# Optimization experiments

Hardware: AMD Instinct MI355X
Metric: run time of the kernel (lower is better)

Reference implementation:

```python
import jax, jax.numpy as jnp
import numpy as np

EPS = 1e-4


def _linear_scan(a, b):
    # y_t = a_t * y_{t-1} + b_t ; a: [L], b: [L, d]
    def combine(c1, c2):
        a1, b1 = c1
        a2, b2 = c2
        return a1 * a2, a2[..., None] * b1 + b2
    _, y = jax.lax.associative_scan(combine, (a, b))
    return y


def setup_inputs() -> dict:
    key = jax.random.key(0)
    k1, k2, k3 = jax.random.split(key, 3)
    L_inner, d, n_seqs = 131072, 512, 8
    h_flat = jax.random.normal(k1, (L_inner, d), dtype=jnp.float32)
    p_selected_flat = jax.random.uniform(k2, (L_inner,), dtype=jnp.float32)
    # outer stream: alternating boundary mask -> cumsum-1 indexes stay in [0, L_inner-1]
    b_flat = jnp.tile(jnp.array([1, 0], dtype=jnp.int32), L_inner)  # [2*L_inner]
    h_seq_idx = jnp.sort(jax.random.randint(k3, (1, L_inner), 0, n_seqs)).astype(jnp.int32)
    return {"h_flat": h_flat, "b_flat": b_flat,
            "p_selected_flat": p_selected_flat, "h_seq_idx": h_seq_idx}


def reference(h_flat, b_flat, p_selected_flat, h_seq_idx):
    # dt derivation: p clamped, dt = -log(1-p); x = h / dt (cast round-trip as in torch)
    p = jnp.clip(p_selected_flat.astype(jnp.float32), EPS, 1.0 - EPS)
    dt = -jnp.log1p(-p)                                   # [L]
    x = (h_flat.astype(jnp.float32) / dt[:, None]).astype(h_flat.dtype).astype(jnp.float32)
    # mamba_chunk_scan_combined with A=-1, B=p, C=1, dstate=1 reduces to:
    #   state_t = exp(-dt_t) * state_{t-1} + dt_t * p_t * x_t ; y_t = state_t
    # with state reset at seq_idx segment boundaries.
    seq = h_seq_idx[0]
    start = jnp.concatenate([jnp.array([True]), seq[1:] != seq[:-1]])
    a = jnp.where(start, 0.0, jnp.exp(-dt))               # decay (== 1-p), reset at starts
    b = (dt * p)[:, None] * x                             # [L, d] input term (== p*h)
    z_bar = _linear_scan(a, b).astype(h_flat.dtype)       # [L_inner, d]
    # dechunk expand: each outer token reads the state of its latest chunk
    idx = jnp.cumsum(b_flat) - 1                          # [L_outer]
    return z_bar[idx]
```

## Files before the change

### kernel.cpp

```cpp
#include <hip/hip_runtime.h>
#include <math.h>

#define EPSV 1e-4f
#define SCHUNK 64

__device__ __forceinline__ float agent_load_f(const float* p) {
    return __hip_atomic_load(p, __ATOMIC_RELAXED, __HIP_MEMORY_SCOPE_AGENT);
}
__device__ __forceinline__ void agent_store_f(float* p, float v) {
    __hip_atomic_store(p, v, __ATOMIC_RELAXED, __HIP_MEMORY_SCOPE_AGENT);
}
__device__ __forceinline__ int agent_load_i(const int* p) {
    return __hip_atomic_load(p, __ATOMIC_RELAXED, __HIP_MEMORY_SCOPE_AGENT);
}
__device__ __forceinline__ void agent_store_i(int* p, int v) {
    __hip_atomic_store(p, v, __ATOMIC_RELAXED, __HIP_MEMORY_SCOPE_AGENT);
}

__global__ void clear_kernel(int* __restrict__ flags, int n) {
    int i = blockIdx.x * blockDim.x + threadIdx.x;
    if (i < n) flags[i] = 0;
}

__global__ void scan_sum_kernel(const int* __restrict__ b, int n,
                                int* __restrict__ bsum) {
    __shared__ int red[256];
    int tid = threadIdx.x;
    int base = blockIdx.x * 1024 + tid * 4;
    int s = 0;
#pragma unroll
    for (int k = 0; k < 4; ++k) {
        int j = base + k;
        if (j < n) s += b[j];
    }
    red[tid] = s;
    __syncthreads();
    for (int off = 128; off > 0; off >>= 1) {
        if (tid < off) red[tid] += red[tid + off];
        __syncthreads();
    }
    if (tid == 0) bsum[blockIdx.x] = red[0];
}

__global__ void scan_offsets_kernel(const int* __restrict__ bsum,
                                    int* __restrict__ boff, int nb) {
    __shared__ int sh[1024];
    int i = threadIdx.x;
    int v = (i < nb) ? bsum[i] : 0;
    sh[i] = v;
    __syncthreads();
    for (int off = 1; off < 1024; off <<= 1) {
        int t = sh[i];
        if (i >= off) t += sh[i - off];
        __syncthreads();
        sh[i] = t;
        __syncthreads();
    }
    if (i < nb) boff[i] = sh[i] - v;
}

__global__ void scan_emit_kernel(const int* __restrict__ b, int n,
                                 const int* __restrict__ boff,
                                 int* __restrict__ sidx, int L, int Louter) {
    __shared__ int red[256];
    int tid = threadIdx.x;
    int base = blockIdx.x * 1024 + tid * 4;
    int v[4];
    int s = 0;
#pragma unroll
    for (int k = 0; k < 4; ++k) {
        int j = base + k;
        v[k] = (j < n) ? b[j] : 0;
        s += v[k];
    }
    red[tid] = s;
    __syncthreads();
    for (int off = 1; off < 256; off <<= 1) {
        int t = red[tid];
        if (tid >= off) t += red[tid - off];
        __syncthreads();
        red[tid] = t;
        __syncthreads();
    }
    int cum = red[tid] - s + boff[blockIdx.x];
#pragma unroll
    for (int k = 0; k < 4; ++k) {
        int j = base + k;
        if (j < n) {
            cum += v[k];
            if (v[k] > 0) {
                int t = cum - 1;
                if (t >= 0 && t < L) sidx[t] = j;
            }
        }
    }
    if (base == 0 && blockIdx.x == 0) sidx[L] = Louter;
}

__global__ __launch_bounds__(512, 4) void scan_lookback_kernel(
        const float* __restrict__ h,
        const float* __restrict__ psel,
        const int* __restrict__ seq,
        const int* __restrict__ sidx,
        float* __restrict__ out,
        float* __restrict__ aggE,
        float* __restrict__ aggP,
        int* __restrict__ flags,
        int L, int d, int Louter, int NC) {
    __shared__ float sh_a[SCHUNK];
    __shared__ float sh_p[SCHUNK];
    __shared__ int   sh_j[SCHUNK + 1];
    __shared__ int   sh_g;
    __shared__ float sh_Pown;
    __shared__ float sh_Pbr;

    const int tid = threadIdx.x;
    if (tid == 0) sh_g = atomicAdd(&flags[NC], 1);
    __syncthreads();
    const int g  = sh_g;
    const int t0 = g * SCHUNK;
    const int nt = min(SCHUNK, L - t0);

    if (tid < nt) {
        int t = t0 + tid;
        float p = psel[t];
        p = fminf(fmaxf(p, EPSV), 1.0f - EPSV);
        bool start = (t == 0) || (seq[t] != seq[t - 1]);
        sh_a[tid] = start ? 0.0f : (1.0f - p);
        sh_p[tid] = p;
    }
    if (tid <= nt) sh_j[tid] = sidx[t0 + tid];
    __syncthreads();

    if (tid < 64) {
        float v = (tid < nt) ? sh_a[tid] : 1.0f;
#pragma unroll
        for (int m = 1; m < 64; m <<= 1) v *= __shfl_xor(v, m);
        if (tid == 0) sh_Pown = v;
    }

    const int c = tid;
    const float* __restrict__ hp = h + (size_t)t0 * d + c;

    float st = 0.0f;
    const bool full = (nt == SCHUNK);
    if (full) {
#pragma unroll
        for (int grp = 0; grp < SCHUNK / 8; ++grp) {
            float hb[8];
#pragma unroll
            for (int k = 0; k < 8; ++k)
                hb[k] = hp[(size_t)(grp * 8 + k) * d];
#pragma unroll
            for (int k = 0; k < 8; ++k) {
                int t = grp * 8 + k;
                st = fmaf(sh_a[t], st, sh_p[t] * hb[k]);
            }
        }
    } else {
        for (int t = 0; t < nt; ++t)
            st = fmaf(sh_a[t], st, sh_p[t] * hp[(size_t)t * d]);
    }

    agent_store_f(&aggE[(size_t)g * d + c], st);
    __syncthreads();
    if (tid == 0) {
        agent_store_f(&aggP[g], sh_Pown);
        asm volatile("s_waitcnt vmcnt(0)" ::: "memory");
        agent_store_i(&flags[g], 1);
    }

    float carry = 0.0f;
    float prodAcc = 1.0f;
    for (int i = g - 1; i >= 0; --i) {
        if (tid == 0) {
            while (agent_load_i(&flags[i]) == 0) __builtin_amdgcn_s_sleep(1);
            sh_Pbr = agent_load_f(&aggP[i]);
        }
        __syncthreads();
        float Pi = sh_Pbr;
        carry = fmaf(prodAcc, agent_load_f(&aggE[(size_t)i * d + c]), carry);
        prodAcc *= Pi;
        __syncthreads();
        if (prodAcc == 0.0f) break;
    }

    float s2 = carry;
    if (full) {
#pragma unroll
        for (int grp = 0; grp < SCHUNK / 8; ++grp) {
            float hb[8];
#pragma unroll
            for (int k = 0; k < 8; ++k)
                hb[k] = hp[(size_t)(grp * 8 + k) * d];
#pragma unroll
            for (int k = 0; k < 8; ++k) {
                int t = grp * 8 + k;
                s2 = fmaf(sh_a[t], s2, sh_p[t] * hb[k]);
                int j0 = max(sh_j[t], 0);
                int j1 = min(sh_j[t + 1], Louter);
                for (int j = j0; j < j1; ++j)
                    __builtin_nontemporal_store(s2, out + (size_t)j * d + c);
            }
        }
    } else {
        for (int t = 0; t < nt; ++t) {
            s2 = fmaf(sh_a[t], s2, sh_p[t] * hp[(size_t)t * d]);
            int j0 = max(sh_j[t], 0);
            int j1 = min(sh_j[t + 1], Louter);
            for (int j = j0; j < j1; ++j)
                out[(size_t)j * d + c] = s2;
        }
    }
}

extern "C" void kernel_launch(void* const* d_in, const int* in_sizes, int n_in,
                              void* d_out, int out_size, void* d_ws, size_t ws_size,
                              hipStream_t stream) {
    const float* h     = (const float*)d_in[0];
    const int*   bflat = (const int*)d_in[1];
    const float* psel  = (const float*)d_in[2];
    const int*   seq   = (const int*)d_in[3];
    float* out = (float*)d_out;

    const int L      = in_sizes[2];
    const int Louter = in_sizes[1];
    const int d      = in_sizes[0] / L;

    const int NC = (L + SCHUNK - 1) / SCHUNK;
    const int nb = (Louter + 1023) / 1024;

    char* ws = (char*)d_ws;
    size_t off = 0;
    auto alloc = [&](size_t bytes) -> void* {
        void* p = ws + off;
        off = (off + bytes + 255) & ~(size_t)255;
        return p;
    };
    float* aggE  = (float*)alloc((size_t)NC * d * 4);
    float* aggP  = (float*)alloc((size_t)NC * 4);
    int*   flags = (int*)alloc((size_t)(NC + 1) * 4);
    int*   bsum  = (int*)alloc((size_t)nb * 4);
    int*   boff  = (int*)alloc((size_t)nb * 4);
    int*   sidx  = (int*)alloc((size_t)(L + 1) * 4);
    (void)ws_size;

    clear_kernel<<<(NC + 1 + 255) / 256, 256, 0, stream>>>(flags, NC + 1);

    scan_sum_kernel<<<nb, 256, 0, stream>>>(bflat, Louter, bsum);
    scan_offsets_kernel<<<1, 1024, 0, stream>>>(bsum, boff, nb);
    scan_emit_kernel<<<nb, 256, 0, stream>>>(bflat, Louter, boff, sidx, L, Louter);

    scan_lookback_kernel<<<NC, d, 0, stream>>>(h, psel, seq, sidx, out,
                                               aggE, aggP, flags,
                                               L, d, Louter, NC);
}
```

Measured before the change: 190.0 us.

## Vectorize lookback scan to float4 per thread and fuse index scan kernels

```diff
diff --git a/kernel.cpp b/kernel.cpp
--- a/kernel.cpp
+++ b/kernel.cpp
@@ -4,6 +4,8 @@
 #define EPSV 1e-4f
 #define SCHUNK 64
 
+typedef float f32x4 __attribute__((ext_vector_type(4)));
+
 __device__ __forceinline__ float agent_load_f(const float* p) {
     return __hip_atomic_load(p, __ATOMIC_RELAXED, __HIP_MEMORY_SCOPE_AGENT);
 }
@@ -15,6 +17,14 @@
 }
 __device__ __forceinline__ void agent_store_i(int* p, int v) {
     __hip_atomic_store(p, v, __ATOMIC_RELAXED, __HIP_MEMORY_SCOPE_AGENT);
+}
+__device__ __forceinline__ f32x4 agent_load_f4(const float* p) {
+    f32x4 r;
+    r.x = agent_load_f(p + 0);
+    r.y = agent_load_f(p + 1);
+    r.z = agent_load_f(p + 2);
+    r.w = agent_load_f(p + 3);
+    return r;
 }
 
 __global__ void clear_kernel(int* __restrict__ flags, int n) {
@@ -22,49 +32,17 @@
     if (i < n) flags[i] = 0;
 }
 
-__global__ void scan_sum_kernel(const int* __restrict__ b, int n,
-                                int* __restrict__ bsum) {
+__global__ __launch_bounds__(256) void sidx_kernel(
+        const int* __restrict__ b, int n,
+        int* __restrict__ bsum,
+        int* __restrict__ flags2,
+        int* __restrict__ sidx, int L, int Louter) {
     __shared__ int red[256];
-    int tid = threadIdx.x;
-    int base = blockIdx.x * 1024 + tid * 4;
-    int s = 0;
-#pragma unroll
-    for (int k = 0; k < 4; ++k) {
-        int j = base + k;
-        if (j < n) s += b[j];
-    }
-    red[tid] = s;
-    __syncthreads();
-    for (int off = 128; off > 0; off >>= 1) {
-        if (tid < off) red[tid] += red[tid + off];
-        __syncthreads();
-    }
-    if (tid == 0) bsum[blockIdx.x] = red[0];
-}
-
-__global__ void scan_offsets_kernel(const int* __restrict__ bsum,
-                                    int* __restrict__ boff, int nb) {
-    __shared__ int sh[1024];
-    int i = threadIdx.x;
-    int v = (i < nb) ? bsum[i] : 0;
-    sh[i] = v;
-    __syncthreads();
-    for (int off = 1; off < 1024; off <<= 1) {
-        int t = sh[i];
-        if (i >= off) t += sh[i - off];
-        __syncthreads();
-        sh[i] = t;
-        __syncthreads();
-    }
-    if (i < nb) boff[i] = sh[i] - v;
-}
-
-__global__ void scan_emit_kernel(const int* __restrict__ b, int n,
-                                 const int* __restrict__ boff,
-                                 int* __restrict__ sidx, int L, int Louter) {
-    __shared__ int red[256];
-    int tid = threadIdx.x;
-    int base = blockIdx.x * 1024 + tid * 4;
+    __shared__ int red2[256];
+    const int tid = threadIdx.x;
+    const int bid = blockIdx.x;
+    const int base = bid * 1024 + tid * 4;
+
     int v[4];
     int s = 0;
 #pragma unroll
@@ -82,7 +60,25 @@
         red[tid] = t;
         __syncthreads();
     }
-    int cum = red[tid] - s + boff[blockIdx.x];
+    if (tid == 255) {
+        agent_store_i(&bsum[bid], red[255]);
+        asm volatile("s_waitcnt vmcnt(0)" ::: "memory");
+        agent_store_i(&flags2[bid], 1);
+    }
+    int mysum = 0;
+    if (tid < bid) {
+        while (agent_load_i(&flags2[tid]) == 0) __builtin_amdgcn_s_sleep(1);
+        mysum = agent_load_i(&bsum[tid]);
+    }
+    red2[tid] = mysum;
+    __syncthreads();
+    for (int off = 128; off > 0; off >>= 1) {
+        if (tid < off) red2[tid] += red2[tid + off];
+        __syncthreads();
+    }
+    const int boff = red2[0];
+
+    int cum = red[tid] - s + boff;
 #pragma unroll
     for (int k = 0; k < 4; ++k) {
         int j = base + k;
@@ -94,10 +90,10 @@
             }
         }
     }
-    if (base == 0 && blockIdx.x == 0) sidx[L] = Louter;
-}
-
-__global__ __launch_bounds__(512, 4) void scan_lookback_kernel(
+    if (tid == 0 && bid == 0) sidx[L] = Louter;
+}
+
+__global__ __launch_bounds__(128, 4) void scan_lookback_kernel(
         const float* __restrict__ h,
         const float* __restrict__ psel,
         const int* __restrict__ seq,
@@ -139,30 +135,44 @@
         if (tid == 0) sh_Pown = v;
     }
 
-    const int c = tid;
-    const float* __restrict__ hp = h + (size_t)t0 * d + c;
-
-    float st = 0.0f;
+    const int c0 = tid * 4;
+    const float* __restrict__ hp = h + (size_t)t0 * d + c0;
+
+    f32x4 st = {0.f, 0.f, 0.f, 0.f};
     const bool full = (nt == SCHUNK);
     if (full) {
 #pragma unroll
         for (int grp = 0; grp < SCHUNK / 8; ++grp) {
-            float hb[8];
+            f32x4 hb[8];
 #pragma unroll
             for (int k = 0; k < 8; ++k)
-                hb[k] = hp[(size_t)(grp * 8 + k) * d];
+                hb[k] = *(const f32x4*)(hp + (size_t)(grp * 8 + k) * d);
 #pragma unroll
             for (int k = 0; k < 8; ++k) {
                 int t = grp * 8 + k;
-                st = fmaf(sh_a[t], st, sh_p[t] * hb[k]);
+                float at = sh_a[t], pt = sh_p[t];
+                st.x = fmaf(at, st.x, pt * hb[k].x);
+                st.y = fmaf(at, st.y, pt * hb[k].y);
+                st.z = fmaf(at, st.z, pt * hb[k].z);
+                st.w = fmaf(at, st.w, pt * hb[k].w);
             }
         }
     } else {
-        for (int t = 0; t < nt; ++t)
-            st = fmaf(sh_a[t], st, sh_p[t] * hp[(size_t)t * d]);
-    }
-
-    agent_store_f(&aggE[(size_t)g * d + c], st);
+        for (int t = 0; t < nt; ++t) {
+            f32x4 h4 = *(const f32x4*)(hp + (size_t)t * d);
+            float at = sh_a[t], pt = sh_p[t];
+            st.x = fmaf(at, st.x, pt * h4.x);
+            st.y = fmaf(at, st.y, pt * h4.y);
+            st.z = fmaf(at, st.z, pt * h4.z);
+            st.w = fmaf(at, st.w, pt * h4.w);
+        }
+    }
+
+    float* ep = aggE + (size_t)g * d + c0;
+    agent_store_f(ep + 0, st.x);
+    agent_store_f(ep + 1, st.y);
+    agent_store_f(ep + 2, st.z);
+    agent_store_f(ep + 3, st.w);
     __syncthreads();
     if (tid == 0) {
         agent_store_f(&aggP[g], sh_Pown);
@@ -170,7 +180,7 @@
         agent_store_i(&flags[g], 1);
     }
 
-    float carry = 0.0f;
+    f32x4 carry = {0.f, 0.f, 0.f, 0.f};
     float prodAcc = 1.0f;
     for (int i = g - 1; i >= 0; --i) {
         if (tid == 0) {
@@ -179,37 +189,50 @@
         }
         __syncthreads();
         float Pi = sh_Pbr;
-        carry = fmaf(prodAcc, agent_load_f(&aggE[(size_t)i * d + c]), carry);
+        f32x4 E = agent_load_f4(aggE + (size_t)i * d + c0);
+        carry.x = fmaf(prodAcc, E.x, carry.x);
+        carry.y = fmaf(prodAcc, E.y, carry.y);
+        carry.z = fmaf(prodAcc, E.z, carry.z);
+        carry.w = fmaf(prodAcc, E.w, carry.w);
         prodAcc *= Pi;
         __syncthreads();
         if (prodAcc == 0.0f) break;
     }
 
-    float s2 = carry;
+    f32x4 s2 = carry;
     if (full) {
 #pragma unroll
         for (int grp = 0; grp < SCHUNK / 8; ++grp) {
-            float hb[8];
+            f32x4 hb[8];
 #pragma unroll
             for (int k = 0; k < 8; ++k)
-                hb[k] = hp[(size_t)(grp * 8 + k) * d];
+                hb[k] = *(const f32x4*)(hp + (size_t)(grp * 8 + k) * d);
 #pragma unroll
             for (int k = 0; k < 8; ++k) {
                 int t = grp * 8 + k;
-                s2 = fmaf(sh_a[t], s2, sh_p[t] * hb[k]);
+                float at = sh_a[t], pt = sh_p[t];
+                s2.x = fmaf(at, s2.x, pt * hb[k].x);
+                s2.y = fmaf(at, s2.y, pt * hb[k].y);
+                s2.z = fmaf(at, s2.z, pt * hb[k].z);
+                s2.w = fmaf(at, s2.w, pt * hb[k].w);
                 int j0 = max(sh_j[t], 0);
                 int j1 = min(sh_j[t + 1], Louter);
                 for (int j = j0; j < j1; ++j)
-                    __builtin_nontemporal_store(s2, out + (size_t)j * d + c);
+                    __builtin_nontemporal_store(s2, (f32x4*)(out + (size_t)j * d + c0));
             }
         }
     } else {
         for (int t = 0; t < nt; ++t) {
-            s2 = fmaf(sh_a[t], s2, sh_p[t] * hp[(size_t)t * d]);
+            f32x4 h4 = *(const f32x4*)(hp + (size_t)t * d);
+            float at = sh_a[t], pt = sh_p[t];
+            s2.x = fmaf(at, s2.x, pt * h4.x);
+            s2.y = fmaf(at, s2.y, pt * h4.y);
+            s2.z = fmaf(at, s2.z, pt * h4.z);
+            s2.w = fmaf(at, s2.w, pt * h4.w);
             int j0 = max(sh_j[t], 0);
             int j1 = min(sh_j[t + 1], Louter);
             for (int j = j0; j < j1; ++j)
-                out[(size_t)j * d + c] = s2;
+                *(f32x4*)(out + (size_t)j * d + c0) = s2;
         }
     }
 }
@@ -237,21 +260,19 @@
         off = (off + bytes + 255) & ~(size_t)255;
         return p;
     };
-    float* aggE  = (float*)alloc((size_t)NC * d * 4);
-    float* aggP  = (float*)alloc((size_t)NC * 4);
-    int*   flags = (int*)alloc((size_t)(NC + 1) * 4);
-    int*   bsum  = (int*)alloc((size_t)nb * 4);
-    int*   boff  = (int*)alloc((size_t)nb * 4);
-    int*   sidx  = (int*)alloc((size_t)(L + 1) * 4);
+    float* aggE   = (float*)alloc((size_t)NC * d * 4);
+    float* aggP   = (float*)alloc((size_t)NC * 4);
+    int*   flags  = (int*)alloc((size_t)(NC + 1 + nb) * 4);
+    int*   bsum   = (int*)alloc((size_t)nb * 4);
+    int*   sidx   = (int*)alloc((size_t)(L + 1) * 4);
+    int*   flags2 = flags + NC + 1;
     (void)ws_size;
 
-    clear_kernel<<<(NC + 1 + 255) / 256, 256, 0, stream>>>(flags, NC + 1);
-
-    scan_sum_kernel<<<nb, 256, 0, stream>>>(bflat, Louter, bsum);
-    scan_offsets_kernel<<<1, 1024, 0, stream>>>(bsum, boff, nb);
-    scan_emit_kernel<<<nb, 256, 0, stream>>>(bflat, Louter, boff, sidx, L, Louter);
-
-    scan_lookback_kernel<<<NC, d, 0, stream>>>(h, psel, seq, sidx, out,
-                                               aggE, aggP, flags,
-                                               L, d, Louter, NC);
-}
+    clear_kernel<<<(NC + 1 + nb + 255) / 256, 256, 0, stream>>>(flags, NC + 1 + nb);
+
+    sidx_kernel<<<nb, 256, 0, stream>>>(bflat, Louter, bsum, flags2, sidx, L, Louter);
+
+    scan_lookback_kernel<<<NC, d / 4, 0, stream>>>(h, psel, seq, sidx, out,
+                                                   aggE, aggP, flags,
+                                                   L, d, Louter, NC);
+}
```

Measured after the change: 215.0 us. 13.2% more time.

## Shrink scan chunk and keep local states in registers to skip second h pass

Applied to the files above, without the earlier changes.

```diff
diff --git a/kernel.cpp b/kernel.cpp
--- a/kernel.cpp
+++ b/kernel.cpp
@@ -2,7 +2,7 @@
 #include <math.h>
 
 #define EPSV 1e-4f
-#define SCHUNK 64
+#define SCHUNK 16
 
 __device__ __forceinline__ float agent_load_f(const float* p) {
     return __hip_atomic_load(p, __ATOMIC_RELAXED, __HIP_MEMORY_SCOPE_AGENT);
@@ -97,7 +97,7 @@
     if (base == 0 && blockIdx.x == 0) sidx[L] = Louter;
 }
 
-__global__ __launch_bounds__(512, 4) void scan_lookback_kernel(
+__global__ __launch_bounds__(512, 8) void scan_lookback_kernel(
         const float* __restrict__ h,
         const float* __restrict__ psel,
         const int* __restrict__ seq,
@@ -109,9 +109,9 @@
         int L, int d, int Louter, int NC) {
     __shared__ float sh_a[SCHUNK];
     __shared__ float sh_p[SCHUNK];
+    __shared__ float sh_A[SCHUNK];
     __shared__ int   sh_j[SCHUNK + 1];
     __shared__ int   sh_g;
-    __shared__ float sh_Pown;
     __shared__ float sh_Pbr;
 
     const int tid = threadIdx.x;
@@ -131,31 +131,28 @@
     }
     if (tid <= nt) sh_j[tid] = sidx[t0 + tid];
     __syncthreads();
-
-    if (tid < 64) {
-        float v = (tid < nt) ? sh_a[tid] : 1.0f;
-#pragma unroll
-        for (int m = 1; m < 64; m <<= 1) v *= __shfl_xor(v, m);
-        if (tid == 0) sh_Pown = v;
-    }
+    if (tid < nt) {
+        float prod = 1.0f;
+        for (int u = 0; u <= tid; ++u) prod *= sh_a[u];
+        sh_A[tid] = prod;
+    }
+    __syncthreads();
 
     const int c = tid;
     const float* __restrict__ hp = h + (size_t)t0 * d + c;
-
+    const bool full = (nt == SCHUNK);
+
+    float z[SCHUNK];
     float st = 0.0f;
-    const bool full = (nt == SCHUNK);
     if (full) {
-#pragma unroll
-        for (int grp = 0; grp < SCHUNK / 8; ++grp) {
-            float hb[8];
-#pragma unroll
-            for (int k = 0; k < 8; ++k)
-                hb[k] = hp[(size_t)(grp * 8 + k) * d];
-#pragma unroll
-            for (int k = 0; k < 8; ++k) {
-                int t = grp * 8 + k;
-                st = fmaf(sh_a[t], st, sh_p[t] * hb[k]);
-            }
+        float hb[SCHUNK];
+#pragma unroll
+        for (int t = 0; t < SCHUNK; ++t)
+            hb[t] = __builtin_nontemporal_load(hp + (size_t)t * d);
+#pragma unroll
+        for (int t = 0; t < SCHUNK; ++t) {
+            st = fmaf(sh_a[t], st, sh_p[t] * hb[t]);
+            z[t] = st;
         }
     } else {
         for (int t = 0; t < nt; ++t)
@@ -165,7 +162,7 @@
     agent_store_f(&aggE[(size_t)g * d + c], st);
     __syncthreads();
     if (tid == 0) {
-        agent_store_f(&aggP[g], sh_Pown);
+        agent_store_f(&aggP[g], sh_A[nt - 1]);
         asm volatile("s_waitcnt vmcnt(0)" ::: "memory");
         agent_store_i(&flags[g], 1);
     }
@@ -185,25 +182,17 @@
         if (prodAcc == 0.0f) break;
     }
 
-    float s2 = carry;
     if (full) {
 #pragma unroll
-        for (int grp = 0; grp < SCHUNK / 8; ++grp) {
-            float hb[8];
-#pragma unroll
-            for (int k = 0; k < 8; ++k)
-                hb[k] = hp[(size_t)(grp * 8 + k) * d];
-#pragma unroll
-            for (int k = 0; k < 8; ++k) {
-                int t = grp * 8 + k;
-                s2 = fmaf(sh_a[t], s2, sh_p[t] * hb[k]);
-                int j0 = max(sh_j[t], 0);
-                int j1 = min(sh_j[t + 1], Louter);
-                for (int j = j0; j < j1; ++j)
-                    __builtin_nontemporal_store(s2, out + (size_t)j * d + c);
-            }
+        for (int t = 0; t < SCHUNK; ++t) {
+            float y = fmaf(sh_A[t], carry, z[t]);
+            int j0 = max(sh_j[t], 0);
+            int j1 = min(sh_j[t + 1], Louter);
+            for (int j = j0; j < j1; ++j)
+                __builtin_nontemporal_store(y, out + (size_t)j * d + c);
         }
     } else {
+        float s2 = carry;
         for (int t = 0; t < nt; ++t) {
             s2 = fmaf(sh_a[t], s2, sh_p[t] * hp[(size_t)t * d]);
             int j0 = max(sh_j[t], 0);
```

Result: slower. 216.0 us (+13.7%).
